# Performance work log

Measured on AMD Instinct MI355X. Metric: run time of the kernel, lower is better.

## Reference

```python
import jax, jax.numpy as jnp
import numpy as np

N_NODES = 4000
N_EDGES = 4000
D_IN = 20      # data_length
HID = 768      # hidden_dim
OUT = 2        # output_dim


def _lin(k, i, o):
    s = 1.0 / np.sqrt(i)
    return jax.random.uniform(k, (i, o), jnp.float32, -s, s)


def setup_inputs() -> dict:
    key = jax.random.key(0)
    ks = jax.random.split(key, 16)
    T = N_NODES + N_EDGES
    data = jax.random.normal(ks[0], (N_NODES, D_IN), jnp.float32)
    data_mask = jnp.ones((N_NODES,), jnp.float32)  # unused by forward, kept for signature fidelity
    e_adj_matrix = jax.random.uniform(ks[1], (T, T), jnp.float32) * (2.0 / T)
    transition = jax.random.randint(ks[2], (2, N_EDGES), 0, N_NODES)
    # exactly N_EDGES ones interleaved among N_NODES zeros
    inx = jnp.concatenate([jnp.ones((N_EDGES,), jnp.int32), jnp.zeros((N_NODES,), jnp.int32)])
    label_inx_positive = jax.random.permutation(ks[3], inx)
    label_inx = jax.random.randint(ks[4], (T,), 0, OUT)
    mask = jax.random.randint(ks[5], (T,), 0, 2).astype(jnp.float32)
    return {
        'data': data, 'data_mask': data_mask, 'e_adj_matrix': e_adj_matrix,
        'transition': transition, 'label_inx_positive': label_inx_positive,
        'label_inx': label_inx, 'mask': mask,
        'mlp_w1': _lin(ks[6], 6 * D_IN, HID), 'mlp_b1': jnp.zeros((HID,), jnp.float32),
        'mlp_w2': _lin(ks[7], HID, HID), 'mlp_b2': jnp.zeros((HID,), jnp.float32),
        'mlp2_w1': _lin(ks[8], D_IN, HID), 'mlp2_b1': jnp.zeros((HID,), jnp.float32),
        'mlp2_w2': _lin(ks[9], HID, HID), 'mlp2_b2': jnp.zeros((HID,), jnp.float32),
        'gcn_w1': _lin(ks[10], HID, HID), 'gcn_b1': jnp.zeros((HID,), jnp.float32),
        'gcn_w2': _lin(ks[11], HID, OUT), 'gcn_b2': jnp.zeros((OUT,), jnp.float32),
    }


def gen_edge2(x, trans):
    # Vectorized Gen_edge2: e1 = [x[t1], x[t0]]; e2 = [x[t0], x[t1]] iff reverse edge exists; e3 = e1 + e2.
    t0, t1 = trans[0], trans[1]
    n = x.shape[0]
    keys = t0 * n + t1
    rkeys = t1 * n + t0
    sk = jnp.sort(keys)
    pos = jnp.clip(jnp.searchsorted(sk, rkeys), 0, sk.shape[0] - 1)
    has_rev = sk[pos] == rkeys  # [E]
    e1 = jnp.concatenate([x[t1], x[t0]], axis=1)  # [E, 2d]
    e2 = jnp.where(has_rev[:, None], jnp.concatenate([x[t0], x[t1]], axis=1), 0.0)
    return jnp.concatenate([e1, e2, e1 + e2], axis=1)  # [E, 6d]


def dataset_cgraph(n_feat, e_feat, e_inx):
    # Vectorized interleave: pull next edge row where e_inx==1, else next node row.
    m = e_inx == 1
    idx_e = jnp.clip(jnp.cumsum(m.astype(jnp.int32)) - 1, 0, e_feat.shape[0] - 1)
    idx_n = jnp.clip(jnp.cumsum((~m).astype(jnp.int32)) - 1, 0, n_feat.shape[0] - 1)
    return jnp.where(m[:, None], e_feat[idx_e], n_feat[idx_n])  # [N+E, H]


def reference(data, data_mask, e_adj_matrix, transition, label_inx_positive,
              label_inx, mask, mlp_w1, mlp_b1, mlp_w2, mlp_b2,
              mlp2_w1, mlp2_b1, mlp2_w2, mlp2_b2,
              gcn_w1, gcn_b1, gcn_w2, gcn_b2):
    e_feat = gen_edge2(data, transition)                              # [E, 120]
    e_feat = jax.nn.relu(e_feat @ mlp_w1 + mlp_b1) @ mlp_w2 + mlp_b2  # [E, H]
    n_feat = jax.nn.relu(data @ mlp2_w1 + mlp2_b1) @ mlp2_w2 + mlp2_b2  # [N, H]
    x = dataset_cgraph(n_feat, e_feat, label_inx_positive)            # [N+E, H]
    # 2-layer GCN (GcnModel assumed standard: relu(A X W1), then A H W2)
    h1 = jax.nn.relu(e_adj_matrix @ (x @ gcn_w1) + gcn_b1)            # [N+E, H]
    logits = e_adj_matrix @ (h1 @ gcn_w2) + gcn_b2                    # [N+E, OUT]
    logp = jax.nn.log_softmax(logits, axis=-1)
    ce = -jnp.take_along_axis(logp, label_inx[:, None], axis=1)[:, 0]
    loss = jnp.sum(ce * mask) / jnp.maximum(jnp.sum(mask), 1.0)
    return logits, loss, h1
```

## Files before the change

kernel.cpp:

```cpp
#include <hip/hip_runtime.h>
#include <hip/hip_bf16.h>

#define N_NODES 4000
#define N_EDGES 4000
#define T_ALL   8000
#define HID     768

typedef __attribute__((ext_vector_type(8))) short bf16x8;
typedef __attribute__((ext_vector_type(4))) short s16x4;
typedef __attribute__((ext_vector_type(4))) float f32x4;

__device__ __forceinline__ short f2bf(float f) {
    union { float f; unsigned u; } a; a.f = f;
    unsigned u = a.u;
    unsigned r = (u + 0x7fffu + ((u >> 16) & 1u)) >> 16;
    return (short)(r & 0xffffu);
}
__device__ __forceinline__ float bf2f(short s) {
    union { unsigned u; float f; } a;
    a.u = ((unsigned)(unsigned short)s) << 16;
    return a.f;
}
__device__ __forceinline__ void gload_lds16(const void* g, void* l) {
    __builtin_amdgcn_global_load_lds(
        (const __attribute__((address_space(1))) void*)g,
        (__attribute__((address_space(3))) void*)l, 16, 0, 0);
}

__global__ __launch_bounds__(512, 2) void gemm_ring(
    const short* __restrict__ A, const short* __restrict__ BT,
    short* __restrict__ parts, int M, int K, int lda, int ldbt)
{
    __shared__ __align__(16) short As[4][256 * 32];
    __shared__ __align__(16) short Bs[4][256 * 32];
    const int t    = threadIdx.x;
    const int lane = t & 63;
    const int wv   = t >> 6;
    const int wm   = wv >> 2;
    const int wn   = wv & 3;
    const int lrow = lane & 15;
    const int kgrp = lane >> 4;

    const int nwg  = gridDim.x * gridDim.y * gridDim.z;
    int flat = blockIdx.x + gridDim.x * (blockIdx.y + gridDim.y * blockIdx.z);
    int w    = (flat & 7) * (nwg >> 3) + (flat >> 3);
    const int bx = w % 3;
    int rest = w / 3;
    const int by = rest & 31;
    const int bz = rest >> 5;
    const int bm0 = by << 8;
    const int bn0 = bx << 8;

    const int TC = K >> 5;
    const int Z  = gridDim.z;
    const int q  = TC / Z, r = TC % Z;
    const int nt   = q + (bz < r ? 1 : 0);
    const int kbeg = ((bz < r) ? bz * (q + 1) : r * (q + 1) + (bz - r) * q) << 5;

    auto stageA = [&](int tt) {
        const int k0 = kbeg + (tt << 5);
        short* dst = &As[tt & 3][0];
#pragma unroll
        for (int i = 0; i < 2; ++i) {
            int f = t + (i << 9);
            int row = f >> 2, sl = f & 3;
            int ga = bm0 + row; ga = ga < M ? ga : M - 1;
            gload_lds16(A + (size_t)ga * lda + k0 + ((sl ^ ((row >> 1) & 3)) << 3),
                        dst + f * 8);
        }
    };
    auto stageB = [&](int tt) {
        const int k0 = kbeg + (tt << 5);
        short* dst = &Bs[tt & 3][0];
#pragma unroll
        for (int i = 0; i < 2; ++i) {
            int f = t + (i << 9);
            int row = f >> 2, sl = f & 3;
            gload_lds16(BT + (size_t)(bn0 + row) * ldbt + k0 + ((sl ^ ((row >> 1) & 3)) << 3),
                        dst + f * 8);
        }
    };

    f32x4 acc[8][4];
#pragma unroll
    for (int m = 0; m < 8; ++m)
#pragma unroll
        for (int n = 0; n < 4; ++n) acc[m][n] = (f32x4)(0.0f);

    stageA(0); stageB(0);
    stageA(1); stageB(1);
    stageA(2); stageB(2);

    for (int tt = 0; tt < nt; ++tt) {
        int ahead = nt - 1 - tt;
        if (ahead >= 2)      asm volatile("s_waitcnt vmcnt(8)" ::: "memory");
        else if (ahead == 1) asm volatile("s_waitcnt vmcnt(4)" ::: "memory");
        else                 asm volatile("s_waitcnt vmcnt(0)" ::: "memory");
        __builtin_amdgcn_sched_barrier(0);
        __builtin_amdgcn_s_barrier();

        if (tt + 3 < nt) { stageA(tt + 3); stageB(tt + 3); }

        const short* Ac = &As[tt & 3][0];
        const short* Bc = &Bs[tt & 3][0];
        bf16x8 af[8], bfv[4];
#pragma unroll
        for (int m = 0; m < 8; ++m) {
            int rr = (wm << 7) + (m << 4) + lrow;
            af[m] = *reinterpret_cast<const bf16x8*>(
                &Ac[(rr << 5) + ((kgrp ^ ((rr >> 1) & 3)) << 3)]);
        }
#pragma unroll
        for (int n = 0; n < 4; ++n) {
            int rr = (wn << 6) + (n << 4) + lrow;
            bfv[n] = *reinterpret_cast<const bf16x8*>(
                &Bc[(rr << 5) + ((kgrp ^ ((rr >> 1) & 3)) << 3)]);
        }
        __builtin_amdgcn_s_setprio(1);
#pragma unroll
        for (int m = 0; m < 8; ++m)
#pragma unroll
            for (int n = 0; n < 4; ++n)
                acc[m][n] = __builtin_amdgcn_mfma_f32_16x16x32_bf16(
                    af[m], bfv[n], acc[m][n], 0, 0, 0);
        __builtin_amdgcn_s_setprio(0);
    }

    short* Cp = parts + (size_t)bz * 6144000;
#pragma unroll
    for (int m = 0; m < 8; ++m) {
        int r0 = bm0 + (wm << 7) + (m << 4) + (kgrp << 2);
#pragma unroll
        for (int n = 0; n < 4; ++n) {
            int col = bn0 + (wn << 6) + (n << 4) + lrow;
#pragma unroll
            for (int j = 0; j < 4; ++j) {
                int rr = r0 + j;
                if (rr < M) Cp[(size_t)rr * 768 + col] = f2bf(acc[m][n][j]);
            }
        }
    }
}

template<int BIAS, int RELU, int OUTBF, int AF32>
__global__ __launch_bounds__(256) void gemm_bf(
    const void* __restrict__ Av, const short* __restrict__ BT,
    const float* __restrict__ bias, void* __restrict__ Cv,
    int M, int N, int K, int lda, int ldbt, int ldc)
{
    __shared__ __align__(16) short As[2][128 * 64];
    __shared__ __align__(16) short Bs[2][128 * 64];
    const int t    = threadIdx.x;
    const int lane = t & 63;
    const int wave = t >> 6;
    const int wr   = (wave >> 1) << 6;
    const int wc   = (wave & 1) << 6;
    const int lrow = lane & 15;
    const int kgrp = lane >> 4;
    const int bm0  = blockIdx.y << 7;
    const int bn0  = blockIdx.x << 7;
    const short* Ab = (const short*)Av;
    const float* Af = (const float*)Av;

    const int nk = K >> 6;

    auto stage = [&](int kt, int buf) {
        const int k0 = kt << 6;
#pragma unroll
        for (int i = 0; i < 4; ++i) {
            int f = t + (i << 8);
            int row = f >> 3, slot = f & 7;
            int gb = bn0 + row; gb = (gb < N) ? gb : (N - 1);
            gload_lds16(BT + (size_t)gb * ldbt + k0 + ((slot ^ (row & 7)) << 3),
                        &Bs[buf][((i << 8) + (wave << 6)) * 8]);
        }
        if constexpr (!AF32) {
#pragma unroll
            for (int i = 0; i < 4; ++i) {
                int f = t + (i << 8);
                int row = f >> 3, slot = f & 7;
                int ga = bm0 + row; ga = (ga < M) ? ga : (M - 1);
                gload_lds16(Ab + (size_t)ga * lda + k0 + ((slot ^ (row & 7)) << 3),
                            &As[buf][((i << 8) + (wave << 6)) * 8]);
            }
        } else {
#pragma unroll
            for (int i = 0; i < 4; ++i) {
                int f = t + (i << 8);
                int row = f >> 3, c8 = f & 7;
                int ga = bm0 + row; ga = (ga < M) ? ga : (M - 1);
                const float* ap = Af + (size_t)ga * lda + k0 + (c8 << 3);
                float4 v0 = *reinterpret_cast<const float4*>(ap);
                float4 v1 = *reinterpret_cast<const float4*>(ap + 4);
                union { bf16x8 v; short s[8]; } u;
                u.s[0] = f2bf(v0.x); u.s[1] = f2bf(v0.y); u.s[2] = f2bf(v0.z); u.s[3] = f2bf(v0.w);
                u.s[4] = f2bf(v1.x); u.s[5] = f2bf(v1.y); u.s[6] = f2bf(v1.z); u.s[7] = f2bf(v1.w);
                *reinterpret_cast<bf16x8*>(&As[buf][row * 64 + ((c8 ^ (row & 7)) << 3)]) = u.v;
            }
        }
    };

    f32x4 acc[4][4];
#pragma unroll
    for (int m = 0; m < 4; ++m)
#pragma unroll
        for (int n = 0; n < 4; ++n) acc[m][n] = (f32x4)(0.0f);

    auto compute = [&](int buf) {
#pragma unroll
        for (int kk = 0; kk < 2; ++kk) {
            bf16x8 af[4], bfv[4];
#pragma unroll
            for (int m = 0; m < 4; ++m) {
                int rr = wr + m * 16 + lrow;
                af[m] = *reinterpret_cast<const bf16x8*>(
                    &As[buf][rr * 64 + (((kk * 4 + kgrp) ^ (rr & 7)) << 3)]);
            }
#pragma unroll
            for (int n = 0; n < 4; ++n) {
                int rr = wc + n * 16 + lrow;
                bfv[n] = *reinterpret_cast<const bf16x8*>(
                    &Bs[buf][rr * 64 + (((kk * 4 + kgrp) ^ (rr & 7)) << 3)]);
            }
#pragma unroll
            for (int m = 0; m < 4; ++m)
#pragma unroll
                for (int n = 0; n < 4; ++n)
                    acc[m][n] = __builtin_amdgcn_mfma_f32_16x16x32_bf16(
                        af[m], bfv[n], acc[m][n], 0, 0, 0);
        }
    };

    if constexpr (!AF32) {
        stage(0, 0);
        if (nk > 1) stage(1, 1);
        for (int kt = 0; kt < nk - 1; ++kt) {
            asm volatile("s_waitcnt vmcnt(8)" ::: "memory");
            __builtin_amdgcn_s_barrier();
            compute(kt & 1);
            __builtin_amdgcn_s_barrier();
            if (kt + 2 < nk) stage(kt + 2, kt & 1);
        }
        asm volatile("s_waitcnt vmcnt(0)" ::: "memory");
        __builtin_amdgcn_s_barrier();
        compute((nk - 1) & 1);
    } else {
        stage(0, 0);
        __syncthreads();
        int cur = 0;
        for (int kt = 0; kt < nk; ++kt) {
            if (kt + 1 < nk) stage(kt + 1, cur ^ 1);
            compute(cur);
            __syncthreads();
            cur ^= 1;
        }
    }

    short* Cb = (short*)Cv;
    float* Cf = (float*)Cv;
#pragma unroll
    for (int m = 0; m < 4; ++m) {
        int rbase = bm0 + wr + m * 16 + kgrp * 4;
#pragma unroll
        for (int n = 0; n < 4; ++n) {
            int col = bn0 + wc + n * 16 + lrow;
            if (col >= N) continue;
            float bv = BIAS ? bias[col] : 0.0f;
#pragma unroll
            for (int j = 0; j < 4; ++j) {
                int rr = rbase + j;
                if (rr < M) {
                    float v = acc[m][n][j] + bv;
                    if (RELU) v = fmaxf(v, 0.0f);
                    if (OUTBF) Cb[(size_t)rr * ldc + col] = f2bf(v);
                    else       Cf[(size_t)rr * ldc + col] = v;
                }
            }
        }
    }
}

template<int RELU>
__global__ __launch_bounds__(256) void gemm_sel(
    const short* __restrict__ A,
    const short* __restrict__ BT1, const short* __restrict__ BT2,
    const float* __restrict__ bias1, const float* __restrict__ bias2,
    short* __restrict__ C, int K)
{
    __shared__ __align__(16) short As[2][128 * 64];
    __shared__ __align__(16) short Bs[2][128 * 64];
    const int t    = threadIdx.x;
    const int lane = t & 63;
    const int wave = t >> 6;
    const int wr   = (wave >> 1) << 6;
    const int wc   = (wave & 1) << 6;
    const int lrow = lane & 15;
    const int kgrp = lane >> 4;
    const int bm0  = blockIdx.y << 7;
    const int bn0  = blockIdx.x << 7;
    const short* BT   = (bm0 < 4096) ? BT1 : BT2;
    const float* bias = (bm0 < 4096) ? bias1 : bias2;
    const int nk = K >> 6;

    auto stage = [&](int kt, int buf) {
        const int k0 = kt << 6;
#pragma unroll
        for (int i = 0; i < 4; ++i) {
            int f = t + (i << 8);
            int row = f >> 3, slot = f & 7;
            gload_lds16(BT + (size_t)(bn0 + row) * K + k0 + ((slot ^ (row & 7)) << 3),
                        &Bs[buf][((i << 8) + (wave << 6)) * 8]);
        }
#pragma unroll
        for (int i = 0; i < 4; ++i) {
            int f = t + (i << 8);
            int row = f >> 3, slot = f & 7;
            gload_lds16(A + (size_t)(bm0 + row) * K + k0 + ((slot ^ (row & 7)) << 3),
                        &As[buf][((i << 8) + (wave << 6)) * 8]);
        }
    };

    f32x4 acc[4][4];
#pragma unroll
    for (int m = 0; m < 4; ++m)
#pragma unroll
        for (int n = 0; n < 4; ++n) acc[m][n] = (f32x4)(0.0f);

    auto compute = [&](int buf) {
#pragma unroll
        for (int kk = 0; kk < 2; ++kk) {
            bf16x8 af[4], bfv[4];
#pragma unroll
            for (int m = 0; m < 4; ++m) {
                int rr = wr + m * 16 + lrow;
                af[m] = *reinterpret_cast<const bf16x8*>(
                    &As[buf][rr * 64 + (((kk * 4 + kgrp) ^ (rr & 7)) << 3)]);
            }
#pragma unroll
            for (int n = 0; n < 4; ++n) {
                int rr = wc + n * 16 + lrow;
                bfv[n] = *reinterpret_cast<const bf16x8*>(
                    &Bs[buf][rr * 64 + (((kk * 4 + kgrp) ^ (rr & 7)) << 3)]);
            }
#pragma unroll
            for (int m = 0; m < 4; ++m)
#pragma unroll
                for (int n = 0; n < 4; ++n)
                    acc[m][n] = __builtin_amdgcn_mfma_f32_16x16x32_bf16(
                        af[m], bfv[n], acc[m][n], 0, 0, 0);
        }
    };

    stage(0, 0);
    if (nk > 1) stage(1, 1);
    for (int kt = 0; kt < nk - 1; ++kt) {
        asm volatile("s_waitcnt vmcnt(8)" ::: "memory");
        __builtin_amdgcn_s_barrier();
        compute(kt & 1);
        __builtin_amdgcn_s_barrier();
        if (kt + 2 < nk) stage(kt + 2, kt & 1);
    }
    asm volatile("s_waitcnt vmcnt(0)" ::: "memory");
    __builtin_amdgcn_s_barrier();
    compute((nk - 1) & 1);

#pragma unroll
    for (int m = 0; m < 4; ++m) {
        int rbase = bm0 + wr + m * 16 + kgrp * 4;
#pragma unroll
        for (int n = 0; n < 4; ++n) {
            int col = bn0 + wc + n * 16 + lrow;
            float bv = bias[col];
#pragma unroll
            for (int j = 0; j < 4; ++j) {
                float v = acc[m][n][j] + bv;
                if (RELU) v = fmaxf(v, 0.0f);
                C[(size_t)(rbase + j) * 768 + col] = f2bf(v);
            }
        }
    }
}

__global__ __launch_bounds__(192) void reduce_h1_hw(
    const short* __restrict__ p, const float* __restrict__ bias,
    const float* __restrict__ w2, float* __restrict__ h1, float* __restrict__ hw,
    int Z)
{
    int r = blockIdx.x, t = threadIdx.x;
    int c0 = t * 4;
    size_t base = (size_t)r * 768 + c0;
    float a[4];
#pragma unroll
    for (int j = 0; j < 4; ++j) a[j] = bias[c0 + j];
    for (int z = 0; z < Z; ++z) {
        s16x4 v = *reinterpret_cast<const s16x4*>(p + (size_t)z * 6144000 + base);
#pragma unroll
        for (int j = 0; j < 4; ++j) a[j] += bf2f(v[j]);
    }
    float d0 = 0.0f, d1 = 0.0f;
    float4 o;
#pragma unroll
    for (int j = 0; j < 4; ++j) {
        float v = fmaxf(a[j], 0.0f);
        ((float*)&o)[j] = v;
        d0 += v * w2[(c0 + j) * 2];
        d1 += v * w2[(c0 + j) * 2 + 1];
    }
    *reinterpret_cast<float4*>(h1 + base) = o;
#pragma unroll
    for (int off = 32; off > 0; off >>= 1) {
        d0 += __shfl_down(d0, off);
        d1 += __shfl_down(d1, off);
    }
    __shared__ float s0[3], s1[3];
    int wvv = t >> 6, ln = t & 63;
    if (ln == 0) { s0[wvv] = d0; s1[wvv] = d1; }
    __syncthreads();
    if (t == 0) {
        hw[r * 2]     = s0[0] + s0[1] + s0[2];
        hw[r * 2 + 1] = s1[0] + s1[1] + s1[2];
    }
}


__global__ void transpose_pad_bf(const float* __restrict__ in, short* __restrict__ out,
                                 int K, int N, int Kp)
{
    int i = blockIdx.x * 256 + threadIdx.x;
    if (i >= N * Kp) return;
    int n = i / Kp, k = i % Kp;
    out[i] = (k < K) ? f2bf(in[k * N + n]) : (short)0;
}

__global__ __launch_bounds__(256) void transpose_f2b(const float* __restrict__ in,
                                                     short* __restrict__ out, int R, int C)
{
    __shared__ float tile[32][33];
    int c0 = blockIdx.x << 5, r0 = blockIdx.y << 5;
    int tx = threadIdx.x & 31, ty = threadIdx.x >> 5;
#pragma unroll
    for (int i = ty; i < 32; i += 8)
        tile[i][tx] = in[(size_t)(r0 + i) * C + c0 + tx];
    __syncthreads();
#pragma unroll
    for (int i = ty; i < 32; i += 8)
        out[(size_t)(c0 + i) * R + r0 + tx] = f2bf(tile[tx][i]);
}

__global__ void cvt_bf16(const float* __restrict__ in, short* __restrict__ out, int n8)
{
    int i = blockIdx.x * 256 + threadIdx.x;
    if (i >= n8) return;
    float4 v0 = *reinterpret_cast<const float4*>(in + (size_t)i * 8);
    float4 v1 = *reinterpret_cast<const float4*>(in + (size_t)i * 8 + 4);
    union { bf16x8 v; short s[8]; } u;
    u.s[0] = f2bf(v0.x); u.s[1] = f2bf(v0.y); u.s[2] = f2bf(v0.z); u.s[3] = f2bf(v0.w);
    u.s[4] = f2bf(v1.x); u.s[5] = f2bf(v1.y); u.s[6] = f2bf(v1.z); u.s[7] = f2bf(v1.w);
    *reinterpret_cast<bf16x8*>(out + (size_t)i * 8) = u.v;
}

__global__ void has_rev_kernel(const int* __restrict__ trans, int* __restrict__ hr, int E)
{
    int e = blockIdx.x;
    int a = trans[e], b = trans[E + e];
    __shared__ int found;
    if (threadIdx.x == 0) found = 0;
    __syncthreads();
    for (int j = threadIdx.x; j < E; j += blockDim.x)
        if (trans[j] == b && trans[E + j] == a) found = 1;
    __syncthreads();
    if (threadIdx.x == 0) hr[e] = found;
}

__global__ void build_eraw(const float* __restrict__ data, const int* __restrict__ trans,
                           const int* __restrict__ hr, short* __restrict__ eraw, int E)
{
    int e = blockIdx.x, c = threadIdx.x;
    int t0 = trans[e], t1 = trans[E + e];
    short* r = eraw + (size_t)e * 128;
    if (c < 20) {
        float x0 = data[t0 * 20 + c];
        float x1 = data[t1 * 20 + c];
        float h  = hr[e] ? 1.0f : 0.0f;
        r[c]       = f2bf(x1);
        r[20 + c]  = f2bf(x0);
        r[40 + c]  = f2bf(h * x0);
        r[60 + c]  = f2bf(h * x1);
        r[80 + c]  = f2bf(x1 + h * x0);
        r[100 + c] = f2bf(x0 + h * x1);
    } else if (c < 28) {
        r[120 + (c - 20)] = 0;
    }
}

__global__ void pad_data(const float* __restrict__ data, short* __restrict__ dp, int Nn)
{
    int i = blockIdx.x * 256 + threadIdx.x;
    if (i >= Nn * 128) return;
    int r = i >> 7, c = i & 127;
    dp[i] = (c < 20) ? f2bf(data[r * 20 + c]) : (short)0;
}

__global__ void build_src(const int* __restrict__ einx, int* __restrict__ src, int T)
{
    __shared__ int partial[256];
    __shared__ int excl[256];
    int t = threadIdx.x;
    int base = t * 32;
    int cnt = 0;
    for (int i = 0; i < 32; ++i) {
        int idx = base + i;
        if (idx < T) cnt += (einx[idx] == 1);
    }
    partial[t] = cnt;
    __syncthreads();
    if (t == 0) {
        int s = 0;
        for (int i = 0; i < 256; ++i) { excl[i] = s; s += partial[i]; }
    }
    __syncthreads();
    int ce = excl[t];
    int cn = base - ce;
    for (int i = 0; i < 32; ++i) {
        int idx = base + i;
        if (idx >= T) break;
        if (einx[idx] == 1) { src[idx] = N_NODES + ce; ce++; }
        else                { src[idx] = cn; cn++; }
    }
}

__global__ void gather_x(const short* __restrict__ nfeat, const short* __restrict__ efeat,
                         const int* __restrict__ src, short* __restrict__ x)
{
    int i = blockIdx.x * 256 + threadIdx.x;
    int r = i / 96, c = i % 96;
    int s = src[r];
    const bf16x8* rowp = (s >= N_NODES)
        ? reinterpret_cast<const bf16x8*>(efeat + (size_t)(s - N_NODES) * HID)
        : reinterpret_cast<const bf16x8*>(nfeat + (size_t)s * HID);
    reinterpret_cast<bf16x8*>(x)[i] = rowp[c];
}

__global__ void h1w2_kernel(const float* __restrict__ h1, const float* __restrict__ w2,
                            float* __restrict__ hw)
{
    int wave = threadIdx.x >> 6, lane = threadIdx.x & 63;
    int row = blockIdx.x * 4 + wave;
    const float* hp = h1 + (size_t)row * HID;
    float a0 = 0.0f, a1 = 0.0f;
    for (int k = lane; k < HID; k += 64) {
        float h = hp[k];
        a0 += h * w2[k * 2];
        a1 += h * w2[k * 2 + 1];
    }
    for (int off = 32; off > 0; off >>= 1) {
        a0 += __shfl_down(a0, off);
        a1 += __shfl_down(a1, off);
    }
    if (lane == 0) { hw[row * 2] = a0; hw[row * 2 + 1] = a1; }
}

__global__ __launch_bounds__(256) void adj_hw_bf(const short* __restrict__ A,
    const float* __restrict__ hw, const float* __restrict__ b2, float* __restrict__ logits)
{
    int row = blockIdx.x;
    const short* ar = A + (size_t)row * T_ALL;
    float a0 = 0.0f, a1 = 0.0f;
    for (int c = threadIdx.x; c < 1000; c += 256) {
        bf16x8 v = *reinterpret_cast<const bf16x8*>(ar + c * 8);
#pragma unroll
        for (int j = 0; j < 8; ++j) {
            float av = bf2f(v[j]);
            int k = c * 8 + j;
            a0 += av * hw[k * 2];
            a1 += av * hw[k * 2 + 1];
        }
    }
    __shared__ float s0[256], s1[256];
    s0[threadIdx.x] = a0; s1[threadIdx.x] = a1;
    __syncthreads();
    for (int o = 128; o > 0; o >>= 1) {
        if (threadIdx.x < o) {
            s0[threadIdx.x] += s0[threadIdx.x + o];
            s1[threadIdx.x] += s1[threadIdx.x + o];
        }
        __syncthreads();
    }
    if (threadIdx.x == 0) {
        logits[row * 2]     = s0[0] + b2[0];
        logits[row * 2 + 1] = s1[0] + b2[1];
    }
}

__global__ __launch_bounds__(256) void adj_hw_f32(const float* __restrict__ A,
    const float* __restrict__ hw, const float* __restrict__ b2, float* __restrict__ logits)
{
    int row = blockIdx.x;
    const float* ar = A + (size_t)row * T_ALL;
    float a0 = 0.0f, a1 = 0.0f;
    for (int k = threadIdx.x; k < T_ALL; k += 256) {
        float v = ar[k];
        a0 += v * hw[k * 2];
        a1 += v * hw[k * 2 + 1];
    }
    __shared__ float s0[256], s1[256];
    s0[threadIdx.x] = a0; s1[threadIdx.x] = a1;
    __syncthreads();
    for (int o = 128; o > 0; o >>= 1) {
        if (threadIdx.x < o) {
            s0[threadIdx.x] += s0[threadIdx.x + o];
            s1[threadIdx.x] += s1[threadIdx.x + o];
        }
        __syncthreads();
    }
    if (threadIdx.x == 0) {
        logits[row * 2]     = s0[0] + b2[0];
        logits[row * 2 + 1] = s1[0] + b2[1];
    }
}

__global__ __launch_bounds__(256) void loss_kernel(const float* __restrict__ logits,
    const int* __restrict__ label, const float* __restrict__ mask, float* __restrict__ outp)
{
    __shared__ float sc[256], sm[256];
    float ac = 0.0f, am = 0.0f;
    for (int i = threadIdx.x; i < T_ALL; i += 256) {
        float l0 = logits[i * 2], l1 = logits[i * 2 + 1];
        float mx = fmaxf(l0, l1);
        float lse = mx + logf(expf(l0 - mx) + expf(l1 - mx));
        float li = label[i] ? l1 : l0;
        ac += (lse - li) * mask[i];
        am += mask[i];
    }
    sc[threadIdx.x] = ac; sm[threadIdx.x] = am;
    __syncthreads();
    for (int o = 128; o > 0; o >>= 1) {
        if (threadIdx.x < o) {
            sc[threadIdx.x] += sc[threadIdx.x + o];
            sm[threadIdx.x] += sm[threadIdx.x + o];
        }
        __syncthreads();
    }
    if (threadIdx.x == 0) *outp = sc[0] / fmaxf(sm[0], 1.0f);
}


extern "C" void kernel_launch(void* const* d_in, const int* in_sizes, int n_in,
                              void* d_out, int out_size, void* d_ws, size_t ws_size,
                              hipStream_t stream)
{
    (void)in_sizes; (void)n_in; (void)out_size;

    const float* data  = (const float*)d_in[0];
    const float* adj   = (const float*)d_in[2];
    const int*   trans = (const int*)d_in[3];
    const int*   einx  = (const int*)d_in[4];
    const int*   label = (const int*)d_in[5];
    const float* mask  = (const float*)d_in[6];
    const float* w1    = (const float*)d_in[7];
    const float* b1    = (const float*)d_in[8];
    const float* w2    = (const float*)d_in[9];
    const float* b2    = (const float*)d_in[10];
    const float* w21   = (const float*)d_in[11];
    const float* b21   = (const float*)d_in[12];
    const float* w22   = (const float*)d_in[13];
    const float* b22   = (const float*)d_in[14];
    const float* gw1   = (const float*)d_in[15];
    const float* gb1   = (const float*)d_in[16];
    const float* gw2   = (const float*)d_in[17];
    const float* gb2   = (const float*)d_in[18];

    char* W = (char*)d_ws;
    short* w1T    = (short*)(W + 0);
    short* w2T    = (short*)(W + 196608);
    short* w21T   = (short*)(W + 1376256);
    short* w22T   = (short*)(W + 1572864);
    short* gw1T   = (short*)(W + 2752512);
    short* estack = (short*)(W + 3932160);
    short* C1s    = (short*)(W + 6029312);
    short* F2s    = (short*)(W + 18612224);
    short* xbuf   = (short*)(W + 31195136);
    int*   hr     = (int*)(W + 43483136);
    int*   src    = (int*)(W + 43499136);

    const bool mid  = (ws_size >= (size_t)140352000);
    const bool big2 = (ws_size >= (size_t)189504000);
    const bool big3 = (ws_size >= (size_t)238656000);
    short* adjbf = (short*)W;
    short* xwT;  float* hwbuf;  short* parts = nullptr;
    if (mid) {
        xwT   = (short*)(W + 128000000);
        hwbuf = (float*)(W + 140288000);
        if (big2) parts = (short*)(W + 140352000);
    } else {
        xwT   = (short*)(W + 48425856);
        hwbuf = (float*)(W + 60713856);
    }

    float* out    = (float*)d_out;
    float* logits = out;
    float* lossp  = out + 16000;
    float* h1     = out + 16001;

    transpose_pad_bf<<<384, 256, 0, stream>>>(w1, w1T, 120, 768, 128);
    transpose_f2b<<<dim3(24, 24), 256, 0, stream>>>(w2, w2T, 768, 768);
    transpose_pad_bf<<<384, 256, 0, stream>>>(w21, w21T, 20, 768, 128);
    transpose_f2b<<<dim3(24, 24), 256, 0, stream>>>(w22, w22T, 768, 768);
    transpose_f2b<<<dim3(24, 24), 256, 0, stream>>>(gw1, gw1T, 768, 768);

    has_rev_kernel<<<4000, 256, 0, stream>>>(trans, hr, N_EDGES);
    build_eraw<<<4000, 32, 0, stream>>>(data, trans, hr, estack, N_EDGES);
    pad_data<<<2000, 256, 0, stream>>>(data, estack + (size_t)4096 * 128, N_NODES);

    gemm_sel<1><<<dim3(6, 64), 256, 0, stream>>>(estack, w1T, w21T, b1, b21, C1s, 128);
    gemm_sel<0><<<dim3(6, 64), 256, 0, stream>>>(C1s, w2T, w22T, b2, b22, F2s, 768);

    build_src<<<1, 256, 0, stream>>>(einx, src, T_ALL);
    gather_x<<<3000, 256, 0, stream>>>(F2s + (size_t)4096 * 768, F2s, src, xbuf);

    gemm_bf<0, 0, 1, 0><<<dim3(63, 6), 256, 0, stream>>>(gw1T, xbuf, nullptr, xwT, 768, 8000, 768, 768, 768, 8000);

    if (mid) {
        cvt_bf16<<<31250, 256, 0, stream>>>(adj, adjbf, 8000000);
        if (big2) {
            const int Z = big3 ? 8 : 4;
            gemm_ring<<<dim3(3, 32, Z), 512, 0, stream>>>(adjbf, xwT, parts, 8000, 8000, 8000, 8000);
            reduce_h1_hw<<<8000, 192, 0, stream>>>(parts, gb1, gw2, h1, hwbuf, Z);
        } else {
            gemm_bf<1, 1, 0, 0><<<dim3(6, 63), 256, 0, stream>>>(adjbf, xwT, gb1, h1, 8000, 768, 8000, 8000, 8000, 768);
            h1w2_kernel<<<2000, 256, 0, stream>>>(h1, gw2, hwbuf);
        }
        adj_hw_bf<<<8000, 256, 0, stream>>>(adjbf, hwbuf, gb2, logits);
    } else {
        gemm_bf<1, 1, 0, 1><<<dim3(6, 63), 256, 0, stream>>>(adj, xwT, gb1, h1, 8000, 768, 8000, 8000, 8000, 768);
        h1w2_kernel<<<2000, 256, 0, stream>>>(h1, gw2, hwbuf);
        adj_hw_f32<<<8000, 256, 0, stream>>>(adj, hwbuf, gb2, logits);
    }
    loss_kernel<<<1, 256, 0, stream>>>(logits, label, mask, lossp);
}
```

Measured before the change: 381.1 us.

## Split ring GEMM K-step into interleaved halves and fuse prep kernels into one launch

The main ring GEMM loop now runs each K-tile in two halves of MFMAs. The A and B prefetch stages are issued separately, one between each half, and the wait-count/barrier logic moves to the end of the iteration. The aim is to overlap global-to-LDS traffic with MFMA work more evenly, at the cost of extra barriers per iteration. Separately, the weight transposes, reverse-edge detection, edge/node feature staging and the src prefix scan are merged into a single prep_all launch, which removes several kernel launches and the hr round trip.

```diff
diff --git a/kernel.cpp b/kernel.cpp
--- a/kernel.cpp
+++ b/kernel.cpp
@@ -90,24 +90,17 @@
     stageA(0); stageB(0);
     stageA(1); stageB(1);
     stageA(2); stageB(2);
+    asm volatile("s_waitcnt vmcnt(8)" ::: "memory");
+    __builtin_amdgcn_s_barrier();
 
     for (int tt = 0; tt < nt; ++tt) {
-        int ahead = nt - 1 - tt;
-        if (ahead >= 2)      asm volatile("s_waitcnt vmcnt(8)" ::: "memory");
-        else if (ahead == 1) asm volatile("s_waitcnt vmcnt(4)" ::: "memory");
-        else                 asm volatile("s_waitcnt vmcnt(0)" ::: "memory");
-        __builtin_amdgcn_sched_barrier(0);
-        __builtin_amdgcn_s_barrier();
-
-        if (tt + 3 < nt) { stageA(tt + 3); stageB(tt + 3); }
-
         const short* Ac = &As[tt & 3][0];
         const short* Bc = &Bs[tt & 3][0];
-        bf16x8 af[8], bfv[4];
-#pragma unroll
-        for (int m = 0; m < 8; ++m) {
+        bf16x8 af0[4], af1[4], bfv[4];
+#pragma unroll
+        for (int m = 0; m < 4; ++m) {
             int rr = (wm << 7) + (m << 4) + lrow;
-            af[m] = *reinterpret_cast<const bf16x8*>(
+            af0[m] = *reinterpret_cast<const bf16x8*>(
                 &Ac[(rr << 5) + ((kgrp ^ ((rr >> 1) & 3)) << 3)]);
         }
 #pragma unroll
@@ -116,14 +109,38 @@
             bfv[n] = *reinterpret_cast<const bf16x8*>(
                 &Bc[(rr << 5) + ((kgrp ^ ((rr >> 1) & 3)) << 3)]);
         }
+        if (tt + 3 < nt) stageA(tt + 3);
+        __builtin_amdgcn_s_barrier();
         __builtin_amdgcn_s_setprio(1);
 #pragma unroll
-        for (int m = 0; m < 8; ++m)
+        for (int m = 0; m < 4; ++m)
 #pragma unroll
             for (int n = 0; n < 4; ++n)
                 acc[m][n] = __builtin_amdgcn_mfma_f32_16x16x32_bf16(
-                    af[m], bfv[n], acc[m][n], 0, 0, 0);
+                    af0[m], bfv[n], acc[m][n], 0, 0, 0);
         __builtin_amdgcn_s_setprio(0);
+        __builtin_amdgcn_s_barrier();
+#pragma unroll
+        for (int m = 0; m < 4; ++m) {
+            int rr = (wm << 7) + 64 + (m << 4) + lrow;
+            af1[m] = *reinterpret_cast<const bf16x8*>(
+                &Ac[(rr << 5) + ((kgrp ^ ((rr >> 1) & 3)) << 3)]);
+        }
+        if (tt + 3 < nt) stageB(tt + 3);
+        __builtin_amdgcn_s_barrier();
+        __builtin_amdgcn_s_setprio(1);
+#pragma unroll
+        for (int m = 0; m < 4; ++m)
+#pragma unroll
+            for (int n = 0; n < 4; ++n)
+                acc[4 + m][n] = __builtin_amdgcn_mfma_f32_16x16x32_bf16(
+                    af1[m], bfv[n], acc[4 + m][n], 0, 0, 0);
+        __builtin_amdgcn_s_setprio(0);
+        int rem = nt - tt;
+        if (rem > 3)       asm volatile("s_waitcnt vmcnt(8)" ::: "memory");
+        else if (rem == 3) asm volatile("s_waitcnt vmcnt(4)" ::: "memory");
+        else if (rem == 2) asm volatile("s_waitcnt vmcnt(0)" ::: "memory");
+        __builtin_amdgcn_s_barrier();
     }
 
     short* Cp = parts + (size_t)bz * 6144000;
@@ -381,6 +398,114 @@
     }
 }
 
+__global__ __launch_bounds__(256) void prep_all(
+    const float* __restrict__ data, const int* __restrict__ trans,
+    const float* __restrict__ w1, const float* __restrict__ w2,
+    const float* __restrict__ w21, const float* __restrict__ w22,
+    const float* __restrict__ gw1, const int* __restrict__ einx,
+    short* __restrict__ w1T, short* __restrict__ w2T,
+    short* __restrict__ w21T, short* __restrict__ w22T,
+    short* __restrict__ gw1T, short* __restrict__ estack,
+    int* __restrict__ src)
+{
+    __shared__ float tile[32][33];
+    __shared__ int ibuf[512];
+    const int blk = blockIdx.x, tid = threadIdx.x;
+
+    if (blk < 2496) {
+        if (blk < 384) {
+            int i = blk * 256 + tid, n = i >> 7, k = i & 127;
+            w1T[i] = (k < 120) ? f2bf(w1[k * 768 + n]) : (short)0;
+        } else if (blk < 1344) {
+            if (blk < 960) {
+                int j = blk - 384, bx = j % 24, by = j / 24;
+                int c0 = bx << 5, r0 = by << 5, tx = tid & 31, ty = tid >> 5;
+#pragma unroll
+                for (int i = ty; i < 32; i += 8)
+                    tile[i][tx] = w2[(size_t)(r0 + i) * 768 + c0 + tx];
+                __syncthreads();
+#pragma unroll
+                for (int i = ty; i < 32; i += 8)
+                    w2T[(size_t)(c0 + i) * 768 + r0 + tx] = f2bf(tile[tx][i]);
+            } else {
+                int i = (blk - 960) * 256 + tid, n = i >> 7, k = i & 127;
+                w21T[i] = (k < 20) ? f2bf(w21[k * 768 + n]) : (short)0;
+            }
+        } else if (blk < 1920) {
+            int j = blk - 1344, bx = j % 24, by = j / 24;
+            int c0 = bx << 5, r0 = by << 5, tx = tid & 31, ty = tid >> 5;
+#pragma unroll
+            for (int i = ty; i < 32; i += 8)
+                tile[i][tx] = w22[(size_t)(r0 + i) * 768 + c0 + tx];
+            __syncthreads();
+#pragma unroll
+            for (int i = ty; i < 32; i += 8)
+                w22T[(size_t)(c0 + i) * 768 + r0 + tx] = f2bf(tile[tx][i]);
+        } else {
+            int j = blk - 1920, bx = j % 24, by = j / 24;
+            int c0 = bx << 5, r0 = by << 5, tx = tid & 31, ty = tid >> 5;
+#pragma unroll
+            for (int i = ty; i < 32; i += 8)
+                tile[i][tx] = gw1[(size_t)(r0 + i) * 768 + c0 + tx];
+            __syncthreads();
+#pragma unroll
+            for (int i = ty; i < 32; i += 8)
+                gw1T[(size_t)(c0 + i) * 768 + r0 + tx] = f2bf(tile[tx][i]);
+        }
+    } else if (blk < 6496) {
+        int e = blk - 2496;
+        int t0 = trans[e], t1 = trans[N_EDGES + e];
+        __shared__ int found;
+        if (tid == 0) found = 0;
+        __syncthreads();
+        for (int j = tid; j < N_EDGES; j += 256)
+            if (trans[j] == t1 && trans[N_EDGES + j] == t0) found = 1;
+        __syncthreads();
+        float h = found ? 1.0f : 0.0f;
+        short* rp = estack + (size_t)e * 128;
+        if (tid < 20) {
+            float x0 = data[t0 * 20 + tid];
+            float x1 = data[t1 * 20 + tid];
+            rp[tid]        = f2bf(x1);
+            rp[20 + tid]   = f2bf(x0);
+            rp[40 + tid]   = f2bf(h * x0);
+            rp[60 + tid]   = f2bf(h * x1);
+            rp[80 + tid]   = f2bf(x1 + h * x0);
+            rp[100 + tid]  = f2bf(x0 + h * x1);
+        } else if (tid < 28) {
+            rp[120 + (tid - 20)] = 0;
+        }
+    } else if (blk < 8496) {
+        int i = (blk - 6496) * 256 + tid;
+        int r = i >> 7, c = i & 127;
+        estack[(size_t)(4096) * 128 + i] = (c < 20) ? f2bf(data[r * 20 + c]) : (short)0;
+    } else {
+        int* partial = ibuf;
+        int* excl    = ibuf + 256;
+        int base = tid * 32;
+        int cnt = 0;
+        for (int i = 0; i < 32; ++i) {
+            int idx = base + i;
+            if (idx < T_ALL) cnt += (einx[idx] == 1);
+        }
+        partial[tid] = cnt;
+        __syncthreads();
+        if (tid == 0) {
+            int s = 0;
+            for (int i = 0; i < 256; ++i) { excl[i] = s; s += partial[i]; }
+        }
+        __syncthreads();
+        int ce = excl[tid];
+        int cn = base - ce;
+        for (int i = 0; i < 32; ++i) {
+            int idx = base + i;
+            if (idx >= T_ALL) break;
+            if (einx[idx] == 1) { src[idx] = N_NODES + ce; ce++; }
+            else                { src[idx] = cn; cn++; }
+        }
+    }
+}
+
 __global__ __launch_bounds__(192) void reduce_h1_hw(
     const short* __restrict__ p, const float* __restrict__ bias,
     const float* __restrict__ w2, float* __restrict__ h1, float* __restrict__ hw,
@@ -422,30 +547,6 @@
     }
 }
 
-
-__global__ void transpose_pad_bf(const float* __restrict__ in, short* __restrict__ out,
-                                 int K, int N, int Kp)
-{
-    int i = blockIdx.x * 256 + threadIdx.x;
-    if (i >= N * Kp) return;
-    int n = i / Kp, k = i % Kp;
-    out[i] = (k < K) ? f2bf(in[k * N + n]) : (short)0;
-}
-
-__global__ __launch_bounds__(256) void transpose_f2b(const float* __restrict__ in,
-                                                     short* __restrict__ out, int R, int C)
-{
-    __shared__ float tile[32][33];
-    int c0 = blockIdx.x << 5, r0 = blockIdx.y << 5;
-    int tx = threadIdx.x & 31, ty = threadIdx.x >> 5;
-#pragma unroll
-    for (int i = ty; i < 32; i += 8)
-        tile[i][tx] = in[(size_t)(r0 + i) * C + c0 + tx];
-    __syncthreads();
-#pragma unroll
-    for (int i = ty; i < 32; i += 8)
-        out[(size_t)(c0 + i) * R + r0 + tx] = f2bf(tile[tx][i]);
-}
 
 __global__ void cvt_bf16(const float* __restrict__ in, short* __restrict__ out, int n8)
 {
@@ -457,76 +558,6 @@
     u.s[0] = f2bf(v0.x); u.s[1] = f2bf(v0.y); u.s[2] = f2bf(v0.z); u.s[3] = f2bf(v0.w);
     u.s[4] = f2bf(v1.x); u.s[5] = f2bf(v1.y); u.s[6] = f2bf(v1.z); u.s[7] = f2bf(v1.w);
     *reinterpret_cast<bf16x8*>(out + (size_t)i * 8) = u.v;
-}
-
-__global__ void has_rev_kernel(const int* __restrict__ trans, int* __restrict__ hr, int E)
-{
-    int e = blockIdx.x;
-    int a = trans[e], b = trans[E + e];
-    __shared__ int found;
-    if (threadIdx.x == 0) found = 0;
-    __syncthreads();
-    for (int j = threadIdx.x; j < E; j += blockDim.x)
-        if (trans[j] == b && trans[E + j] == a) found = 1;
-    __syncthreads();
-    if (threadIdx.x == 0) hr[e] = found;
-}
-
-__global__ void build_eraw(const float* __restrict__ data, const int* __restrict__ trans,
-                           const int* __restrict__ hr, short* __restrict__ eraw, int E)
-{
-    int e = blockIdx.x, c = threadIdx.x;
-    int t0 = trans[e], t1 = trans[E + e];
-    short* r = eraw + (size_t)e * 128;
-    if (c < 20) {
-        float x0 = data[t0 * 20 + c];
-        float x1 = data[t1 * 20 + c];
-        float h  = hr[e] ? 1.0f : 0.0f;
-        r[c]       = f2bf(x1);
-        r[20 + c]  = f2bf(x0);
-        r[40 + c]  = f2bf(h * x0);
-        r[60 + c]  = f2bf(h * x1);
-        r[80 + c]  = f2bf(x1 + h * x0);
-        r[100 + c] = f2bf(x0 + h * x1);
-    } else if (c < 28) {
-        r[120 + (c - 20)] = 0;
-    }
-}
-
-__global__ void pad_data(const float* __restrict__ data, short* __restrict__ dp, int Nn)
-{
-    int i = blockIdx.x * 256 + threadIdx.x;
-    if (i >= Nn * 128) return;
-    int r = i >> 7, c = i & 127;
-    dp[i] = (c < 20) ? f2bf(data[r * 20 + c]) : (short)0;
-}
-
-__global__ void build_src(const int* __restrict__ einx, int* __restrict__ src, int T)
-{
-    __shared__ int partial[256];
-    __shared__ int excl[256];
-    int t = threadIdx.x;
-    int base = t * 32;
-    int cnt = 0;
-    for (int i = 0; i < 32; ++i) {
-        int idx = base + i;
-        if (idx < T) cnt += (einx[idx] == 1);
-    }
-    partial[t] = cnt;
-    __syncthreads();
-    if (t == 0) {
-        int s = 0;
-        for (int i = 0; i < 256; ++i) { excl[i] = s; s += partial[i]; }
-    }
-    __syncthreads();
-    int ce = excl[t];
-    int cn = base - ce;
-    for (int i = 0; i < 32; ++i) {
-        int idx = base + i;
-        if (idx >= T) break;
-        if (einx[idx] == 1) { src[idx] = N_NODES + ce; ce++; }
-        else                { src[idx] = cn; cn++; }
-    }
 }
 
 __global__ void gather_x(const short* __restrict__ nfeat, const short* __restrict__ efeat,
@@ -682,6 +713,7 @@
     short* xbuf   = (short*)(W + 31195136);
     int*   hr     = (int*)(W + 43483136);
     int*   src    = (int*)(W + 43499136);
+    (void)hr;
 
     const bool mid  = (ws_size >= (size_t)140352000);
     const bool big2 = (ws_size >= (size_t)189504000);
@@ -702,20 +734,12 @@
     float* lossp  = out + 16000;
     float* h1     = out + 16001;
 
-    transpose_pad_bf<<<384, 256, 0, stream>>>(w1, w1T, 120, 768, 128);
-    transpose_f2b<<<dim3(24, 24), 256, 0, stream>>>(w2, w2T, 768, 768);
-    transpose_pad_bf<<<384, 256, 0, stream>>>(w21, w21T, 20, 768, 128);
-    transpose_f2b<<<dim3(24, 24), 256, 0, stream>>>(w22, w22T, 768, 768);
-    transpose_f2b<<<dim3(24, 24), 256, 0, stream>>>(gw1, gw1T, 768, 768);
-
-    has_rev_kernel<<<4000, 256, 0, stream>>>(trans, hr, N_EDGES);
-    build_eraw<<<4000, 32, 0, stream>>>(data, trans, hr, estack, N_EDGES);
-    pad_data<<<2000, 256, 0, stream>>>(data, estack + (size_t)4096 * 128, N_NODES);
+    prep_all<<<8497, 256, 0, stream>>>(data, trans, w1, w2, w21, w22, gw1, einx,
+                                       w1T, w2T, w21T, w22T, gw1T, estack, src);
 
     gemm_sel<1><<<dim3(6, 64), 256, 0, stream>>>(estack, w1T, w21T, b1, b21, C1s, 128);
     gemm_sel<0><<<dim3(6, 64), 256, 0, stream>>>(C1s, w2T, w22T, b2, b22, F2s, 768);
 
-    build_src<<<1, 256, 0, stream>>>(einx, src, T_ALL);
     gather_x<<<3000, 256, 0, stream>>>(F2s + (size_t)4096 * 768, F2s, src, xbuf);
 
     gemm_bf<0, 0, 1, 0><<<dim3(63, 6), 256, 0, stream>>>(gw1T, xbuf, nullptr, xwT, 768, 8000, 768, 768, 768, 8000);
```

Measured after the change: 334.3 us. -12.3%, faster.
